# Optimization experiments

Hardware: AMD Instinct MI355X
Metric: run time of the kernel (lower is better)

## Reference

```python
import jax, jax.numpy as jnp
import numpy as np


def setup_inputs() -> dict:
    key = jax.random.key(0)
    k1, k2 = jax.random.split(key)
    B, C, H, W = 8, 64, 128, 256
    src = jax.random.normal(k1, (B, C, H, W), dtype=jnp.float32)
    tgt = jax.random.normal(k2, (B, C, H, W), dtype=jnp.float32)
    return {"src": src, "tgt": tgt, "search_range": 4}


def reference(src, tgt, search_range):
    # Cost volume: for each (dy, dx) shift of tgt (zero-padded), channel dot with src.
    # Output channel ordering matches the torch loop: center, then for i=1..S:
    # (+i,0), (-i,0), (0,+i), (0,-i), then for j=1..S: (+i,+j), (-i,+j), (+i,-j), (-i,-j).
    S = search_range
    B, C, H, W = src.shape
    tgt_pad = jnp.pad(tgt, ((0, 0), (0, 0), (S, S), (S, S)))

    def cost(di, dj):
        # shifted[y, x] = tgt[y - di, x - dj] (zero outside)
        shifted = tgt_pad[:, :, S - di:S - di + H, S - dj:S - dj + W]
        return jnp.sum(shifted * src, axis=1)  # [B, H, W]

    outs = [cost(0, 0)]
    for i in range(1, S + 1):
        outs.extend([cost(i, 0), cost(-i, 0), cost(0, i), cost(0, -i)])
        for j in range(1, S + 1):
            outs.extend([cost(i, j), cost(-i, j), cost(i, -j), cost(-i, -j)])
    return jnp.stack(outs, axis=1)  # [B, (2S+1)^2, H, W]
```

## Files before the change

### kernel.cpp

```cpp
#include <hip/hip_runtime.h>

#define S    4
#define BB   8
#define CC   64
#define HH   128
#define WW   256
#define KCH  16
#define NCP  8
#define TH   8
#define TW   64
#define TROWS 16
#define PITCHD 72
#define NT   768
#define NCH  (CC / KCH)
#define HW   (HH * WW)

typedef _Float16 h2 __attribute__((ext_vector_type(2)));

#if __has_builtin(__builtin_amdgcn_cvt_pkrtz)
__device__ inline h2 pack2(float x, float y) {
  return __builtin_bit_cast(h2, __builtin_amdgcn_cvt_pkrtz(x, y));
}
#else
__device__ inline h2 pack2(float x, float y) { h2 r; r[0] = (_Float16)x; r[1] = (_Float16)y; return r; }
#endif

#if __has_builtin(__builtin_amdgcn_fdot2)
__device__ inline float dot2(h2 a, h2 b, float c) { return __builtin_amdgcn_fdot2(a, b, c, false); }
#else
__device__ inline float dot2(h2 a, h2 b, float c) { return c + (float)a[0]*(float)b[0] + (float)a[1]*(float)b[1]; }
#endif

__device__ __host__ constexpr int ord_idx(int di, int dj) {
  int i = di < 0 ? -di : di;
  int j = dj < 0 ? -dj : dj;
  if (i == 0 && j == 0) return 0;
  if (j == 0) return 1 + (i - 1) * 20 + (di > 0 ? 0 : 1);
  if (i == 0) return 1 + (j - 1) * 20 + (dj > 0 ? 2 : 3);
  return 1 + (i - 1) * 20 + 4 + (j - 1) * 4 +
         (di > 0 ? (dj > 0 ? 0 : 2) : (dj > 0 ? 1 : 3));
}

__global__ __launch_bounds__(NT, 3)
void costvol_kernel(const float* __restrict__ src,
                    const float* __restrict__ tgt,
                    float* __restrict__ out) {
  __shared__ __align__(16) float lds2[NCP * TROWS * PITCHD];

  const int tx  = threadIdx.x;
  const int ty  = threadIdx.y;
  const int tz  = threadIdx.z;
  const int tid = (tz * TH + ty) * 32 + tx;
  const int bx  = blockIdx.x;
  const int by  = blockIdx.y;
  const int b   = blockIdx.z;

  const int w0b = bx * TW;
  const int h0  = by * TH;
  const int h   = h0 + ty;
  const int w0  = w0b + tx * 2;
  const int di_base = tz * 3 - S;

  int lofs[3], goff[3];
#pragma unroll
  for (int k = 0; k < 3; ++k) {
    const int u   = tid + k * NT;
    const int cp  = u / (TROWS * 18);
    const int rem = u - cp * (TROWS * 18);
    const int r   = rem / 18;
    const int wq  = rem - r * 18;
    const int gh  = h0 - S + r;
    const int gw  = w0b - S + 4 * wq;
    lofs[k] = cp * (TROWS * PITCHD) + r * PITCHD + 4 * wq;
    goff[k] = -1;
    if ((unsigned)gh < (unsigned)HH && gw >= 0 && gw + 3 < WW)
      goff[k] = ((b * CC + 2 * cp) * HH + gh) * WW + gw;
  }

  float acc[27][2];
#pragma unroll
  for (int o = 0; o < 27; ++o) { acc[o][0] = 0.f; acc[o][1] = 0.f; }

  const float* srcbase = src + ((size_t)b * CC * HH + h) * WW + w0;

  for (int ch = 0; ch < NCH; ++ch) {
    __syncthreads();

    const int choff = ch * (KCH * HW);
#pragma unroll
    for (int k = 0; k < 3; ++k) {
      float4 va = make_float4(0.f, 0.f, 0.f, 0.f);
      float4 vb = va;
      if (goff[k] >= 0) {
        va = *reinterpret_cast<const float4*>(tgt + goff[k] + choff);
        vb = *reinterpret_cast<const float4*>(tgt + goff[k] + choff + HW);
      }
      float4 wv;
      wv.x = __builtin_bit_cast(float, pack2(va.x, vb.x));
      wv.y = __builtin_bit_cast(float, pack2(va.y, vb.y));
      wv.z = __builtin_bit_cast(float, pack2(va.z, vb.z));
      wv.w = __builtin_bit_cast(float, pack2(va.w, vb.w));
      *reinterpret_cast<float4*>(lds2 + lofs[k]) = wv;
    }

    __syncthreads();

#pragma unroll
    for (int cp = 0; cp < NCP; ++cp) {
      const float* sp = srcbase + (size_t)(ch * KCH + 2 * cp) * HW;
      const float2 sa = *reinterpret_cast<const float2*>(sp);
      const float2 sb = *reinterpret_cast<const float2*>(sp + HW);
      const h2 sp0 = pack2(sa.x, sb.x);
      const h2 sp1 = pack2(sa.y, sb.y);

#pragma unroll
      for (int gi = 0; gi < 3; ++gi) {
        const int row = ty + 8 - 3 * tz - gi;
        const float* lp = lds2 + cp * (TROWS * PITCHD) + row * PITCHD + 2 * tx;
        h2 win[10];
#pragma unroll
        for (int q = 0; q < 5; ++q) {
          const float2 t = *reinterpret_cast<const float2*>(lp + 2 * q);
          win[2 * q]     = __builtin_bit_cast(h2, t.x);
          win[2 * q + 1] = __builtin_bit_cast(h2, t.y);
        }
#pragma unroll
        for (int dj = -S; dj <= S; ++dj) {
          const int o = gi * 9 + (dj + S);
          acc[o][0] = dot2(sp0, win[4 - dj], acc[o][0]);
          acc[o][1] = dot2(sp1, win[5 - dj], acc[o][1]);
        }
      }
    }
  }

  const size_t HWs = (size_t)HW;
  float* op = out + (size_t)b * 81 * HWs + (size_t)h * WW + w0;
#pragma unroll
  for (int gi = 0; gi < 3; ++gi) {
    const int di = di_base + gi;
#pragma unroll
    for (int dj = -S; dj <= S; ++dj) {
      const int o    = ord_idx(di, dj);
      const int slot = gi * 9 + (dj + S);
      *reinterpret_cast<float2*>(op + (size_t)o * HWs) =
          make_float2(acc[slot][0], acc[slot][1]);
    }
  }
}

extern "C" void kernel_launch(void* const* d_in, const int* in_sizes, int n_in,
                              void* d_out, int out_size, void* d_ws, size_t ws_size,
                              hipStream_t stream) {
  const float* src = (const float*)d_in[0];
  const float* tgt = (const float*)d_in[1];
  float* out = (float*)d_out;
  dim3 grid(WW / TW, HH / TH, BB);
  dim3 block(32, TH, 3);
  costvol_kernel<<<grid, block, 0, stream>>>(src, tgt, out);
}
```

Baseline: 75.82 us.

## Split di rows over four thread groups and stage src in LDS as fp16

The block grows from 3 to 4 z-groups, so each thread covers 2 vertical shifts (the last group covers 3) instead of 3, and the launch bound targets 4 blocks. The src channel pairs are now loaded cooperatively once per block, packed to fp16 and kept in LDS. This replaces the redundant per-thread global loads repeated across the z-groups. The aim is to cut accumulator registers and redundant global traffic, at the cost of an uneven per-thread load, a divergent branch on tz, and extra LDS use.

```diff
diff --git a/kernel.cpp b/kernel.cpp
--- a/kernel.cpp
+++ b/kernel.cpp
@@ -11,9 +11,11 @@
 #define TW   64
 #define TROWS 16
 #define PITCHD 72
-#define NT   768
+#define NT   1024
 #define NCH  (CC / KCH)
 #define HW   (HH * WW)
+#define TGTU (NCP * TROWS * 18)
+#define SRCU (NCP * TH * 16)
 
 typedef _Float16 h2 __attribute__((ext_vector_type(2)));
 
@@ -41,11 +43,52 @@
          (di > 0 ? (dj > 0 ? 0 : 2) : (dj > 0 ? 1 : 3));
 }
 
-__global__ __launch_bounds__(NT, 3)
+#define COMPUTE_CHUNK(NGI)                                                   \
+  _Pragma("unroll")                                                          \
+  for (int cp = 0; cp < NCP; ++cp) {                                         \
+    const float2 st = *reinterpret_cast<const float2*>(                      \
+        ldss + (cp * TH + ty) * 64 + 2 * tx);                                \
+    const h2 sp0 = __builtin_bit_cast(h2, st.x);                             \
+    const h2 sp1 = __builtin_bit_cast(h2, st.y);                             \
+    _Pragma("unroll")                                                        \
+    for (int gi = 0; gi < (NGI); ++gi) {                                     \
+      const int row = ty + 8 - 2 * tz - gi;    \
+      const float* lp = lds2 + cp * (TROWS * PITCHD) + row * PITCHD + 2*tx;  \
+      h2 win[10];                                                            \
+      _Pragma("unroll")                                                      \
+      for (int q = 0; q < 5; ++q) {                      \
+        const float2 t = *reinterpret_cast<const float2*>(lp + 2 * q);       \
+        win[2 * q]     = __builtin_bit_cast(h2, t.x);                        \
+        win[2 * q + 1] = __builtin_bit_cast(h2, t.y);                        \
+      }                                                                      \
+      _Pragma("unroll")                                                      \
+      for (int dj = -S; dj <= S; ++dj) {                                     \
+        const int o = gi * 9 + (dj + S);              \
+        acc[o][0] = dot2(sp0, win[4 - dj], acc[o][0]);                       \
+        acc[o][1] = dot2(sp1, win[5 - dj], acc[o][1]);                       \
+      }                                                                      \
+    }                                                                        \
+  }
+
+#define EPILOGUE(NGI)                                                        \
+  _Pragma("unroll")                                                          \
+  for (int gi = 0; gi < (NGI); ++gi) {                                       \
+    const int di = 2 * tz - 4 + gi;                        \
+    _Pragma("unroll")                                                        \
+    for (int dj = -S; dj <= S; ++dj) {                                       \
+      const int o    = ord_idx(di, dj);                                      \
+      const int slot = gi * 9 + (dj + S);                                    \
+      *reinterpret_cast<float2*>(op + (size_t)o * HWs) =                     \
+          make_float2(acc[slot][0], acc[slot][1]);                           \
+    }                                                                        \
+  }
+
+__global__ __launch_bounds__(NT, 4)
 void costvol_kernel(const float* __restrict__ src,
                     const float* __restrict__ tgt,
                     float* __restrict__ out) {
   __shared__ __align__(16) float lds2[NCP * TROWS * PITCHD];
+  __shared__ __align__(16) float ldss[NCP * TH * 64];
 
   const int tx  = threadIdx.x;
   const int ty  = threadIdx.y;
@@ -59,94 +102,77 @@
   const int h0  = by * TH;
   const int h   = h0 + ty;
   const int w0  = w0b + tx * 2;
-  const int di_base = tz * 3 - S;
 
   int lofs[3], goff[3];
 #pragma unroll
   for (int k = 0; k < 3; ++k) {
-    const int u   = tid + k * NT;
-    const int cp  = u / (TROWS * 18);
-    const int rem = u - cp * (TROWS * 18);
-    const int r   = rem / 18;
-    const int wq  = rem - r * 18;
-    const int gh  = h0 - S + r;
-    const int gw  = w0b - S + 4 * wq;
-    lofs[k] = cp * (TROWS * PITCHD) + r * PITCHD + 4 * wq;
-    goff[k] = -1;
-    if ((unsigned)gh < (unsigned)HH && gw >= 0 && gw + 3 < WW)
-      goff[k] = ((b * CC + 2 * cp) * HH + gh) * WW + gw;
+    const int u = tid + k * NT;
+    lofs[k] = -1; goff[k] = -1;
+    if (u < TGTU) {
+      const int cp  = u / (TROWS * 18);
+      const int rem = u - cp * (TROWS * 18);
+      const int r   = rem / 18;
+      const int wq  = rem - r * 18;
+      const int gh  = h0 - S + r;
+      const int gw  = w0b - S + 4 * wq;
+      lofs[k] = cp * (TROWS * PITCHD) + r * PITCHD + 4 * wq;
+      if ((unsigned)gh < (unsigned)HH && gw >= 0 && gw + 3 < WW)
+        goff[k] = ((b * CC + 2 * cp) * HH + gh) * WW + gw;
+    }
   }
+
+  const int scp = tid >> 7;
+  const int sr  = (tid >> 4) & 7;
+  const int sq  = tid & 15;
+  const int sgo = (b * CC + 2 * scp) * HW + (h0 + sr) * WW + w0b + 4 * sq;
+  const int slo = (scp * TH + sr) * 64 + 4 * sq;
 
   float acc[27][2];
 #pragma unroll
   for (int o = 0; o < 27; ++o) { acc[o][0] = 0.f; acc[o][1] = 0.f; }
 
-  const float* srcbase = src + ((size_t)b * CC * HH + h) * WW + w0;
-
   for (int ch = 0; ch < NCH; ++ch) {
     __syncthreads();
 
     const int choff = ch * (KCH * HW);
+
 #pragma unroll
     for (int k = 0; k < 3; ++k) {
-      float4 va = make_float4(0.f, 0.f, 0.f, 0.f);
-      float4 vb = va;
-      if (goff[k] >= 0) {
-        va = *reinterpret_cast<const float4*>(tgt + goff[k] + choff);
-        vb = *reinterpret_cast<const float4*>(tgt + goff[k] + choff + HW);
+      if (lofs[k] >= 0) {
+        float4 va = make_float4(0.f, 0.f, 0.f, 0.f);
+        float4 vb = va;
+        if (goff[k] >= 0) {
+          va = *reinterpret_cast<const float4*>(tgt + goff[k] + choff);
+          vb = *reinterpret_cast<const float4*>(tgt + goff[k] + choff + HW);
+        }
+        float4 wv;
+        wv.x = __builtin_bit_cast(float, pack2(va.x, vb.x));
+        wv.y = __builtin_bit_cast(float, pack2(va.y, vb.y));
+        wv.z = __builtin_bit_cast(float, pack2(va.z, vb.z));
+        wv.w = __builtin_bit_cast(float, pack2(va.w, vb.w));
+        *reinterpret_cast<float4*>(lds2 + lofs[k]) = wv;
       }
+    }
+
+    {
+      const float4 va = *reinterpret_cast<const float4*>(src + sgo + choff);
+      const float4 vb = *reinterpret_cast<const float4*>(src + sgo + choff + HW);
       float4 wv;
       wv.x = __builtin_bit_cast(float, pack2(va.x, vb.x));
       wv.y = __builtin_bit_cast(float, pack2(va.y, vb.y));
       wv.z = __builtin_bit_cast(float, pack2(va.z, vb.z));
       wv.w = __builtin_bit_cast(float, pack2(va.w, vb.w));
-      *reinterpret_cast<float4*>(lds2 + lofs[k]) = wv;
+      *reinterpret_cast<float4*>(ldss + slo) = wv;
     }
 
     __syncthreads();
 
-#pragma unroll
-    for (int cp = 0; cp < NCP; ++cp) {
-      const float* sp = srcbase + (size_t)(ch * KCH + 2 * cp) * HW;
-      const float2 sa = *reinterpret_cast<const float2*>(sp);
-      const float2 sb = *reinterpret_cast<const float2*>(sp + HW);
-      const h2 sp0 = pack2(sa.x, sb.x);
-      const h2 sp1 = pack2(sa.y, sb.y);
-
-#pragma unroll
-      for (int gi = 0; gi < 3; ++gi) {
-        const int row = ty + 8 - 3 * tz - gi;
-        const float* lp = lds2 + cp * (TROWS * PITCHD) + row * PITCHD + 2 * tx;
-        h2 win[10];
-#pragma unroll
-        for (int q = 0; q < 5; ++q) {
-          const float2 t = *reinterpret_cast<const float2*>(lp + 2 * q);
-          win[2 * q]     = __builtin_bit_cast(h2, t.x);
-          win[2 * q + 1] = __builtin_bit_cast(h2, t.y);
-        }
-#pragma unroll
-        for (int dj = -S; dj <= S; ++dj) {
-          const int o = gi * 9 + (dj + S);
-          acc[o][0] = dot2(sp0, win[4 - dj], acc[o][0]);
-          acc[o][1] = dot2(sp1, win[5 - dj], acc[o][1]);
-        }
-      }
-    }
+    if (tz == 3) { COMPUTE_CHUNK(3) } else { COMPUTE_CHUNK(2) }
   }
 
   const size_t HWs = (size_t)HW;
   float* op = out + (size_t)b * 81 * HWs + (size_t)h * WW + w0;
-#pragma unroll
-  for (int gi = 0; gi < 3; ++gi) {
-    const int di = di_base + gi;
-#pragma unroll
-    for (int dj = -S; dj <= S; ++dj) {
-      const int o    = ord_idx(di, dj);
-      const int slot = gi * 9 + (dj + S);
-      *reinterpret_cast<float2*>(op + (size_t)o * HWs) =
-          make_float2(acc[slot][0], acc[slot][1]);
-    }
-  }
+  if (tz == 3) { EPILOGUE(3) } else { EPILOGUE(2) }
 }
 
 extern "C" void kernel_launch(void* const* d_in, const int* in_sizes, int n_in,
@@ -156,6 +182,6 @@
   const float* tgt = (const float*)d_in[1];
   float* out = (float*)d_out;
   dim3 grid(WW / TW, HH / TH, BB);
-  dim3 block(32, TH, 3);
+  dim3 block(32, TH, 4);
   costvol_kernel<<<grid, block, 0, stream>>>(src, tgt, out);
 }
```

Result: no change. 75.24 us (-0.8%).

## Restructure cost-volume tiling: 4 pixels per thread, one dy per thread, src staged in LDS

Applied to the files above, without the earlier changes.

Changes the thread mapping so each thread computes 4 adjacent pixels for a single vertical offset across all 9 horizontal offsets, instead of 2 pixels for 3 vertical offsets. Tile height drops to 4 rows with 9 z-threads, and the source tile is now loaded cooperatively into LDS as packed fp16 rather than read per thread from global memory. The goal is more window reuse per LDS read (float4 loads), wider float4 output stores, fewer redundant global src reads, and higher occupancy. The cost is a larger tgt halo per output row, since each 4-row tile needs 12 rows, and extra LDS space.

```diff
diff --git a/kernel.cpp b/kernel.cpp
--- a/kernel.cpp
+++ b/kernel.cpp
@@ -7,13 +7,17 @@
 #define WW   256
 #define KCH  16
 #define NCP  8
-#define TH   8
+#define TH   4
 #define TW   64
-#define TROWS 16
+#define PX   4
+#define NTX  16
+#define TROWS 12
 #define PITCHD 72
-#define NT   768
+#define NT   576
 #define NCH  (CC / KCH)
 #define HW   (HH * WW)
+#define TGTU (NCP * TROWS * 18)
+#define SRCU (NCP * TH * 16)
 
 typedef _Float16 h2 __attribute__((ext_vector_type(2)));
 
@@ -41,16 +45,17 @@
          (di > 0 ? (dj > 0 ? 0 : 2) : (dj > 0 ? 1 : 3));
 }
 
-__global__ __launch_bounds__(NT, 3)
+__global__ __launch_bounds__(NT, 4)
 void costvol_kernel(const float* __restrict__ src,
                     const float* __restrict__ tgt,
                     float* __restrict__ out) {
   __shared__ __align__(16) float lds2[NCP * TROWS * PITCHD];
+  __shared__ __align__(16) float ldss[NCP * TH * 64];
 
   const int tx  = threadIdx.x;
   const int ty  = threadIdx.y;
   const int tz  = threadIdx.z;
-  const int tid = (tz * TH + ty) * 32 + tx;
+  const int tid = tz * 64 + ty * 16 + tx;
   const int bx  = blockIdx.x;
   const int by  = blockIdx.y;
   const int b   = blockIdx.z;
@@ -58,8 +63,9 @@
   const int w0b = bx * TW;
   const int h0  = by * TH;
   const int h   = h0 + ty;
-  const int w0  = w0b + tx * 2;
-  const int di_base = tz * 3 - S;
+  const int w0  = w0b + tx * PX;
+  const int di  = tz - S;
+  const int row = ty - tz + 8;
 
   int lofs[3], goff[3];
 #pragma unroll
@@ -74,19 +80,26 @@
     lofs[k] = cp * (TROWS * PITCHD) + r * PITCHD + 4 * wq;
     goff[k] = -1;
     if ((unsigned)gh < (unsigned)HH && gw >= 0 && gw + 3 < WW)
-      goff[k] = ((b * CC + 2 * cp) * HH + gh) * WW + gw;
+      goff[k] = ((b * CC + 2 * cp) * HW) + gh * WW + gw;
   }
 
-  float acc[27][2];
+  const int scp = tid >> 6;
+  const int sr  = (tid >> 4) & 3;
+  const int sq  = tid & 15;
+  const int sgo = (b * CC + 2 * scp) * HW + (h0 + sr) * WW + w0b + 4 * sq;
+  const int slo = (scp * TH + sr) * 64 + 4 * sq;
+
+  float acc[9][PX];
 #pragma unroll
-  for (int o = 0; o < 27; ++o) { acc[o][0] = 0.f; acc[o][1] = 0.f; }
-
-  const float* srcbase = src + ((size_t)b * CC * HH + h) * WW + w0;
+  for (int o = 0; o < 9; ++o)
+#pragma unroll
+    for (int p = 0; p < PX; ++p) acc[o][p] = 0.f;
 
   for (int ch = 0; ch < NCH; ++ch) {
     __syncthreads();
 
     const int choff = ch * (KCH * HW);
+
 #pragma unroll
     for (int k = 0; k < 3; ++k) {
       float4 va = make_float4(0.f, 0.f, 0.f, 0.f);
@@ -103,33 +116,42 @@
       *reinterpret_cast<float4*>(lds2 + lofs[k]) = wv;
     }
 
+    if (tid < SRCU) {
+      const float4 va = *reinterpret_cast<const float4*>(src + sgo + choff);
+      const float4 vb = *reinterpret_cast<const float4*>(src + sgo + choff + HW);
+      float4 wv;
+      wv.x = __builtin_bit_cast(float, pack2(va.x, vb.x));
+      wv.y = __builtin_bit_cast(float, pack2(va.y, vb.y));
+      wv.z = __builtin_bit_cast(float, pack2(va.z, vb.z));
+      wv.w = __builtin_bit_cast(float, pack2(va.w, vb.w));
+      *reinterpret_cast<float4*>(ldss + slo) = wv;
+    }
+
     __syncthreads();
 
 #pragma unroll
     for (int cp = 0; cp < NCP; ++cp) {
-      const float* sp = srcbase + (size_t)(ch * KCH + 2 * cp) * HW;
-      const float2 sa = *reinterpret_cast<const float2*>(sp);
-      const float2 sb = *reinterpret_cast<const float2*>(sp + HW);
-      const h2 sp0 = pack2(sa.x, sb.x);
-      const h2 sp1 = pack2(sa.y, sb.y);
+      const float4 st = *reinterpret_cast<const float4*>(
+          ldss + (cp * TH + ty) * 64 + 4 * tx);
+      const h2 sv[PX] = {__builtin_bit_cast(h2, st.x), __builtin_bit_cast(h2, st.y),
+                         __builtin_bit_cast(h2, st.z), __builtin_bit_cast(h2, st.w)};
+
+      const float* lp = lds2 + cp * (TROWS * PITCHD) + row * PITCHD + 4 * tx;
+      h2 win[12];
+#pragma unroll
+      for (int q = 0; q < 3; ++q) {
+        const float4 t = *reinterpret_cast<const float4*>(lp + 4 * q);
+        win[4 * q]     = __builtin_bit_cast(h2, t.x);
+        win[4 * q + 1] = __builtin_bit_cast(h2, t.y);
+        win[4 * q + 2] = __builtin_bit_cast(h2, t.z);
+        win[4 * q + 3] = __builtin_bit_cast(h2, t.w);
+      }
 
 #pragma unroll
-      for (int gi = 0; gi < 3; ++gi) {
-        const int row = ty + 8 - 3 * tz - gi;
-        const float* lp = lds2 + cp * (TROWS * PITCHD) + row * PITCHD + 2 * tx;
-        h2 win[10];
+      for (int dj = -S; dj <= S; ++dj) {
 #pragma unroll
-        for (int q = 0; q < 5; ++q) {
-          const float2 t = *reinterpret_cast<const float2*>(lp + 2 * q);
-          win[2 * q]     = __builtin_bit_cast(h2, t.x);
-          win[2 * q + 1] = __builtin_bit_cast(h2, t.y);
-        }
-#pragma unroll
-        for (int dj = -S; dj <= S; ++dj) {
-          const int o = gi * 9 + (dj + S);
-          acc[o][0] = dot2(sp0, win[4 - dj], acc[o][0]);
-          acc[o][1] = dot2(sp1, win[5 - dj], acc[o][1]);
-        }
+        for (int p = 0; p < PX; ++p)
+          acc[dj + S][p] = dot2(sv[p], win[p - dj + 4], acc[dj + S][p]);
       }
     }
   }
@@ -137,15 +159,11 @@
   const size_t HWs = (size_t)HW;
   float* op = out + (size_t)b * 81 * HWs + (size_t)h * WW + w0;
 #pragma unroll
-  for (int gi = 0; gi < 3; ++gi) {
-    const int di = di_base + gi;
-#pragma unroll
-    for (int dj = -S; dj <= S; ++dj) {
-      const int o    = ord_idx(di, dj);
-      const int slot = gi * 9 + (dj + S);
-      *reinterpret_cast<float2*>(op + (size_t)o * HWs) =
-          make_float2(acc[slot][0], acc[slot][1]);
-    }
+  for (int dj = -S; dj <= S; ++dj) {
+    const int o    = ord_idx(di, dj);
+    const int slot = dj + S;
+    *reinterpret_cast<float4*>(op + (size_t)o * HWs) =
+        make_float4(acc[slot][0], acc[slot][1], acc[slot][2], acc[slot][3]);
   }
 }
 
@@ -156,6 +174,6 @@
   const float* tgt = (const float*)d_in[1];
   float* out = (float*)d_out;
   dim3 grid(WW / TW, HH / TH, BB);
-  dim3 block(32, TH, 3);
+  dim3 block(NTX, TH, 9);
   costvol_kernel<<<grid, block, 0, stream>>>(src, tgt, out);
 }
```

New measurement: 72.69 us. -4.1%, faster.
